# Performance work log

Hardware: AMD Instinct MI355X
Metric: run time of the kernel (lower is better)

The kernel has to match this reference:

```python
import jax, jax.numpy as jnp
import numpy as np

S, N, D, F, L = 16, 64, 1270, 150, 8  # sentences, entities, emb dim, ffnn_size, num_labels


def _xavier(key, shape):
    lim = np.sqrt(6.0 / (shape[0] + shape[1])).astype(np.float32)
    return jax.random.uniform(key, shape, jnp.float32, -lim, lim)


def setup_inputs() -> dict:
    key = jax.random.key(0)
    ks = jax.random.split(key, 8)
    entity_emb = jax.random.normal(ks[0], (S, N, D), jnp.float32)
    entity_scores = jax.random.normal(ks[1], (S, N), jnp.float32)
    rel_labels = jax.random.randint(ks[2], (S, N, N), 0, L)
    num_predicted_entities = jax.random.randint(ks[3], (S,), 0, N)
    # Linear params stored [in, out] (y = x @ W + b), transpose of torch layout.
    W_in = _xavier(ks[4], (3 * D, F))
    b_in = jnp.zeros((F,), jnp.float32)
    W_h = _xavier(ks[5], (F, F))
    b_h = jnp.zeros((F,), jnp.float32)
    W_out = _xavier(ks[6], (F, L - 1))
    b_out = jnp.zeros((L - 1,), jnp.float32)
    return {
        "entity_emb": entity_emb,
        "entity_scores": entity_scores,
        "W_in": W_in, "b_in": b_in,
        "W_h": W_h, "b_h": b_h,
        "W_out": W_out, "b_out": b_out,
        "rel_labels": rel_labels,
        "num_predicted_entities": num_predicted_entities,
    }


def reference(entity_emb, entity_scores, W_in, b_in, W_h, b_h, W_out, b_out,
              rel_labels, num_predicted_entities):
    s, n, d = entity_emb.shape
    # pair_emb = concat([e1_tiled, e2_tiled, e1*e2]) @ W_in  ==  split-weight fused form
    # (avoids materializing the [S,N,N,3D] tensor; same math).
    W1, W2, W3 = W_in[:d], W_in[d:2 * d], W_in[2 * d:]
    h = (jnp.einsum('sid,df->sif', entity_emb, W1)[:, :, None, :]
         + jnp.einsum('sjd,df->sjf', entity_emb, W2)[:, None, :, :]
         + jnp.einsum('sid,sjd,df->sijf', entity_emb, entity_emb, W3)
         + b_in)  # [S,N,N,F]
    # NOTE: original applies two more Linear layers with NO nonlinearity between them.
    h = h @ W_h + b_h
    scores = h @ W_out + b_out  # [S,N,N,L-1]
    # dropout is identity at inference (reference baseline)
    rel = scores + entity_scores[:, :, None, None] + entity_scores[:, None, :, None]
    dummy = jnp.zeros((s, n, n, 1), rel.dtype)
    rel_scores = jnp.concatenate([dummy, rel], axis=3)  # [S,N,N,L]
    # per-element cross entropy (reduction='none'), then pair mask, then sum
    logp = jax.nn.log_softmax(rel_scores, axis=-1)
    ce = -jnp.take_along_axis(logp, rel_labels[..., None], axis=-1)[..., 0]  # [S,N,N]
    ent_mask = jnp.arange(n)[None, :] < num_predicted_entities[:, None]  # [S,N]
    pair_mask = ent_mask[:, :, None] & ent_mask[:, None, :]  # [S,N,N]
    loss = jnp.sum(jnp.where(pair_mask, ce, jnp.zeros((), ce.dtype)))
    return rel_scores, loss
```

## Files before the change

### kernel.cpp

```cpp
#include <hip/hip_runtime.h>
#include <hip/hip_bf16.h>
#include <stdint.h>

typedef __attribute__((ext_vector_type(8))) short bf16x8;
typedef __attribute__((ext_vector_type(16))) float f32x16;

#define S_ 16
#define N_ 64
#define D_ 1270
#define F_ 150
#define KP_ 1280
#define FP_ 160
#define NKT 80
#define LOSS_OFF (S_*N_*N_*8)

#define HSTR 172

__device__ inline short f2b(float x) {
    union { float f; uint32_t u; } v; v.f = x;
    uint32_t r = (v.u + 0x7fffu + ((v.u >> 16) & 1u)) >> 16;
    return (short)r;
}
__device__ inline bf16x8 as_bf16x8(uint4 u) {
    union { uint4 a; bf16x8 b; } c; c.a = u; return c.b;
}

__global__ void k_pack(const float* __restrict__ emb, const float* __restrict__ win,
                       const float* __restrict__ wh, const float* __restrict__ wout,
                       short* __restrict__ eapk, short* __restrict__ w3pk,
                       short* __restrict__ w12pk, short* __restrict__ whpk,
                       short* __restrict__ wopk, float* __restrict__ out) {
    int t = blockIdx.x * 256 + threadIdx.x;
    if (t == 0) out[LOSS_OFF] = 0.f;
    const int TOT_EA = S_ * NKT * 2 * 64;
    const int NW3 = NKT * 5 * 64, NW12 = NKT * 10 * 64, NWH = 10 * 5 * 64, NWO = 10 * 64;
    if (t < TOT_EA) {
        int l  = t & 63;
        int mt = (t >> 6) & 1;
        int kt = (t >> 7) % NKT;
        int s  = t / (NKT * 2 * 64);
        int i  = (l & 31) + mt * 32;
        int k0 = kt * 16 + (l >> 5) * 8;
        const float* src = emb + (size_t)(s * N_ + i) * D_;
        bf16x8 pk;
        if (k0 + 8 <= D_) {
            float2 v0 = *(const float2*)(src + k0);
            float2 v1 = *(const float2*)(src + k0 + 2);
            float2 v2 = *(const float2*)(src + k0 + 4);
            float2 v3 = *(const float2*)(src + k0 + 6);
            pk[0]=f2b(v0.x); pk[1]=f2b(v0.y); pk[2]=f2b(v1.x); pk[3]=f2b(v1.y);
            pk[4]=f2b(v2.x); pk[5]=f2b(v2.y); pk[6]=f2b(v3.x); pk[7]=f2b(v3.y);
        } else {
            #pragma unroll
            for (int u = 0; u < 8; ++u) {
                int k = k0 + u;
                pk[u] = (k < D_) ? f2b(src[k]) : (short)0;
            }
        }
        *(bf16x8*)(eapk + (size_t)t * 8) = pk;
        return;
    }
    int t0 = t - TOT_EA;
    if (t0 < NW3) {
        int l = t0 & 63, nt = (t0 >> 6) % 5, kt = t0 / 320;
        int k0 = kt * 16 + (l >> 5) * 8, f = (l & 31) + nt * 32;
        bf16x8 pk;
        #pragma unroll
        for (int u = 0; u < 8; ++u) {
            int k = k0 + u;
            pk[u] = (k < D_ && f < F_) ? f2b(win[((size_t)(2 * D_) + k) * F_ + f]) : (short)0;
        }
        *(bf16x8*)(w3pk + (size_t)t0 * 8) = pk;
    } else if (t0 < NW3 + NW12) {
        int t2 = t0 - NW3;
        int l = t2 & 63, nt = (t2 >> 6) % 10, kt = t2 / 640;
        int k0 = kt * 16 + (l >> 5) * 8, c = (l & 31) + nt * 32;
        bf16x8 pk;
        #pragma unroll
        for (int u = 0; u < 8; ++u) {
            int k = k0 + u;
            float val = 0.f;
            if (k < D_) {
                if (c < FP_) { if (c < F_) val = win[(size_t)k * F_ + c]; }
                else { int f = c - FP_; if (f < F_) val = win[((size_t)D_ + k) * F_ + f]; }
            }
            pk[u] = f2b(val);
        }
        *(bf16x8*)(w12pk + (size_t)t2 * 8) = pk;
    } else if (t0 < NW3 + NW12 + NWH) {
        int t3 = t0 - NW3 - NW12;
        int l = t3 & 63, nt = (t3 >> 6) % 5, kt = t3 / 320;
        int k0 = kt * 16 + (l >> 5) * 8, f = (l & 31) + nt * 32;
        bf16x8 pk;
        #pragma unroll
        for (int u = 0; u < 8; ++u) {
            int k = k0 + u;
            pk[u] = (k < F_ && f < F_) ? f2b(wh[(size_t)k * F_ + f]) : (short)0;
        }
        *(bf16x8*)(whpk + (size_t)t3 * 8) = pk;
    } else if (t0 < NW3 + NW12 + NWH + NWO) {
        int t4 = t0 - NW3 - NW12 - NWH;
        int l = t4 & 63, kt = t4 >> 6;
        int k0 = kt * 16 + (l >> 5) * 8, f = l & 31;
        bf16x8 pk;
        #pragma unroll
        for (int u = 0; u < 8; ++u) {
            int k = k0 + u;
            pk[u] = (k < F_ && f < 7) ? f2b(wout[k * 7 + f]) : (short)0;
        }
        *(bf16x8*)(wopk + (size_t)t4 * 8) = pk;
    }
}

__global__ __launch_bounds__(128) void k_p12(const short* __restrict__ eapk,
                                             const short* __restrict__ w12pk,
                                             const float* __restrict__ bin,
                                             float* __restrict__ p1, float* __restrict__ p2) {
    __shared__ float red[16][64];
    int bid = blockIdx.x;
    int x = bid & 7, k = bid >> 3;
    int s = x * 2 + (k / 20);
    int rr = k % 20;
    int nt = rr >> 1, mt = rr & 1;
    int lane = threadIdx.x & 63, ks = threadIdx.x >> 6;
    f32x16 acc;
    #pragma unroll
    for (int r = 0; r < 16; ++r) acc[r] = 0.f;
    const size_t abase = (size_t)s * NKT * 2 * 64 * 8;
    #pragma unroll 8
    for (int kt = ks * 40; kt < ks * 40 + 40; ++kt) {
        bf16x8 a = *(const bf16x8*)(eapk + abase + ((size_t)kt * 2 + mt) * 64 * 8 + (size_t)lane * 8);
        bf16x8 b = *(const bf16x8*)(w12pk + ((size_t)(kt * 10 + nt) * 64 + lane) * 8);
        acc = __builtin_amdgcn_mfma_f32_32x32x16_bf16(a, b, acc, 0, 0, 0);
    }
    if (ks == 1) {
        #pragma unroll
        for (int r = 0; r < 16; ++r) red[r][lane] = acc[r];
    }
    __syncthreads();
    if (ks == 0) {
        int c = (lane & 31) + nt * 32;
        #pragma unroll
        for (int r = 0; r < 16; ++r) {
            float v = acc[r] + red[r][lane];
            int i = (r & 3) + 8 * (r >> 2) + 4 * (lane >> 5) + mt * 32;
            if (c < FP_) {
                p1[(size_t)(s * N_ + i) * FP_ + c] = v;
            } else {
                int f = c - FP_;
                float bv = (f < F_) ? bin[f] : 0.f;
                p2[(size_t)(s * N_ + i) * FP_ + f] = v + bv;
            }
        }
    }
}

template<int NB>
__device__ __forceinline__ void run_gemm1(const char* ea, const char* w3,
                                          const float* ej0, f32x16 (&acc)[3]) {
    uint4 euA, euB;
    uint4 bfA[3], bfB[3];
    float4 ejA[2], ejB4[2];

    auto fetch = [&](int kt, uint4& eu, uint4 (&bfv)[3], float4 (&ejr)[2]) {
        eu = *(const uint4*)(ea + (size_t)kt * 2048);
        #pragma unroll
        for (int nb = 0; nb < NB; ++nb)
            bfv[nb] = *(const uint4*)(w3 + (size_t)kt * 5120 + nb * 1024);
        ejr[0] = *(const float4*)(ej0 + kt * 16);
        ejr[1] = *(const float4*)(ej0 + kt * 16 + 4);
    };
    auto step = [&](const uint4& eu, const uint4 (&bfv)[3], const float4 (&ejr)[2]) {
        float ev[8] = {ejr[0].x,ejr[0].y,ejr[0].z,ejr[0].w,ejr[1].x,ejr[1].y,ejr[1].z,ejr[1].w};
        uint32_t ew[4] = {eu.x, eu.y, eu.z, eu.w};
        union { uint32_t u[4]; bf16x8 v; } av;
        #pragma unroll
        for (int p = 0; p < 4; ++p) {
            float flo = __uint_as_float(ew[p] << 16) * ev[2 * p];
            float fhi = __uint_as_float(ew[p] & 0xffff0000u) * ev[2 * p + 1];
            uint32_t pk;
            asm("v_cvt_pk_bf16_f32 %0, %1, %2" : "=v"(pk) : "v"(flo), "v"(fhi));
            av.u[p] = pk;
        }
        #pragma unroll
        for (int nb = 0; nb < NB; ++nb)
            acc[nb] = __builtin_amdgcn_mfma_f32_32x32x16_bf16(av.v, as_bf16x8(bfv[nb]), acc[nb], 0, 0, 0);
    };

    fetch(0, euA, bfA, ejA);
    fetch(1, euB, bfB, ejB4);
    #pragma unroll 1
    for (int kt = 0; kt < NKT; kt += 2) {
        step(euA, bfA, ejA);
        if (kt + 2 < NKT) fetch(kt + 2, euA, bfA, ejA);
        step(euB, bfB, ejB4);
        if (kt + 3 < NKT) fetch(kt + 3, euB, bfB, ejB4);
    }
}

template<int NB, int NT0>
__device__ __forceinline__ void write_h1(const f32x16 (&acc)[3], short* hBj,
                                         const float* p1s, const float* p2r,
                                         int lane, int mt) {
    #pragma unroll
    for (int nb = 0; nb < NB; ++nb) {
        const int f = (lane & 31) + (NT0 + nb) * 32;
        const float p2v = p2r[f];
        #pragma unroll
        for (int r = 0; r < 16; ++r) {
            int i = (r & 3) + 8 * (r >> 2) + 4 * (lane >> 5) + mt * 32;
            hBj[i * HSTR + f] = f2b(acc[nb][r] + p1s[(size_t)i * FP_ + f] + p2v);
        }
    }
}

__global__ __launch_bounds__(512, 1) void k_main(
    const float* __restrict__ emb, const float* __restrict__ esc,
    const short* __restrict__ eapk, const short* __restrict__ w3pk,
    const short* __restrict__ whpk, const short* __restrict__ wopk,
    const float* __restrict__ p1g, const float* __restrict__ p2g,
    const float* __restrict__ bhv, const float* __restrict__ bout,
    const int* __restrict__ labels, const int* __restrict__ nump,
    float* __restrict__ out) {

    __shared__ char lds[48128];
    float* sbuf = (float*)lds;
    float* ejB  = (float*)(lds + 4096);
    short* hB   = (short*)(lds + 4096);

    const int tid = threadIdx.x, lane = tid & 63, w = tid >> 6;
    const int jl = w & 1, mt = (w >> 1) & 1, nh = w >> 2;
    const int hi8 = (lane >> 5) << 3;
    const int bid = blockIdx.x;
    const int x = bid & 7, kk2 = bid >> 3;
    const int s = x * 2 + (kk2 >> 5);
    const int j0 = (kk2 & 31) * 2;

    for (int idx = tid; idx < 2 * KP_; idx += 512) {
        int jr = idx / KP_, k = idx - jr * KP_;
        ejB[idx] = (k < D_) ? emb[(size_t)(s * N_ + j0 + jr) * D_ + k] : 0.f;
    }
    __syncthreads();

    f32x16 acc[3];
    #pragma unroll
    for (int nb = 0; nb < 3; ++nb)
        #pragma unroll
        for (int r = 0; r < 16; ++r) acc[nb][r] = 0.f;

    {
        const char* ea = (const char*)eapk + (size_t)s * 163840 + mt * 1024 + lane * 16;
        const char* w3 = (const char*)w3pk + (nh ? 3 : 0) * 1024 + lane * 16;
        const float* ej0 = ejB + jl * KP_ + hi8;
        if (nh == 0) run_gemm1<3>(ea, w3, ej0, acc);
        else         run_gemm1<2>(ea, w3, ej0, acc);
    }
    __syncthreads();

    {
        const float* p1s = p1g + (size_t)(s * N_) * FP_;
        const float* p2r = p2g + (size_t)(s * N_ + j0 + jl) * FP_;
        short* hBj = hB + jl * (64 * HSTR);
        if (nh == 0) write_h1<3, 0>(acc, hBj, p1s, p2r, lane, mt);
        else         write_h1<2, 3>(acc, hBj, p1s, p2r, lane, mt);
    }
    __syncthreads();

    f32x16 acc2[3];
    #pragma unroll
    for (int c = 0; c < 3; ++c)
        #pragma unroll
        for (int r = 0; r < 16; ++r) acc2[c][r] = 0.f;
    #pragma unroll 1
    for (int kt = 0; kt < 10; ++kt) {
        #pragma unroll
        for (int c = 0; c < 3; ++c) {
            int t = w + 8 * c;
            if (t >= 20) break;
            int jl2 = t / 10, tt = t % 10;
            int mt2 = tt / 5, nt2 = tt % 5;
            const short* ap = hB + jl2 * (64 * HSTR) + ((lane & 31) + mt2 * 32) * HSTR
                            + kt * 16 + hi8;
            short4 alo = *(const short4*)ap;
            short4 ahi = *(const short4*)(ap + 4);
            union { short sh[8]; bf16x8 v; } av;
            av.sh[0] = alo.x; av.sh[1] = alo.y; av.sh[2] = alo.z; av.sh[3] = alo.w;
            av.sh[4] = ahi.x; av.sh[5] = ahi.y; av.sh[6] = ahi.z; av.sh[7] = ahi.w;
            bf16x8 b = *(const bf16x8*)(whpk + ((size_t)(kt * 5 + nt2) * 64 + lane) * 8);
            acc2[c] = __builtin_amdgcn_mfma_f32_32x32x16_bf16(av.v, b, acc2[c], 0, 0, 0);
        }
    }
    __syncthreads();

    #pragma unroll
    for (int c = 0; c < 3; ++c) {
        int t = w + 8 * c;
        if (t >= 20) break;
        int jl2 = t / 10, tt = t % 10;
        int mt2 = tt / 5, nt2 = tt % 5;
        int f = (lane & 31) + nt2 * 32;
        float bhf = (f < F_) ? bhv[f] : 0.f;
        #pragma unroll
        for (int r = 0; r < 16; ++r) {
            int i = (r & 3) + 8 * (r >> 2) + 4 * (lane >> 5) + mt2 * 32;
            short hv = (f < F_) ? f2b(acc2[c][r] + bhf) : (short)0;
            hB[jl2 * (64 * HSTR) + i * HSTR + f] = hv;
        }
    }
    __syncthreads();

    if (w < 4) {
        int jl3 = w >> 1, mt3 = w & 1;
        f32x16 acc3;
        #pragma unroll
        for (int r = 0; r < 16; ++r) acc3[r] = 0.f;
        #pragma unroll 1
        for (int kt = 0; kt < 10; ++kt) {
            const short* ap = hB + jl3 * (64 * HSTR) + ((lane & 31) + mt3 * 32) * HSTR
                            + kt * 16 + hi8;
            short4 alo = *(const short4*)ap;
            short4 ahi = *(const short4*)(ap + 4);
            union { short sh[8]; bf16x8 v; } av;
            av.sh[0] = alo.x; av.sh[1] = alo.y; av.sh[2] = alo.z; av.sh[3] = alo.w;
            av.sh[4] = ahi.x; av.sh[5] = ahi.y; av.sh[6] = ahi.z; av.sh[7] = ahi.w;
            bf16x8 b = *(const bf16x8*)(wopk + ((size_t)(kt * 64) + lane) * 8);
            acc3 = __builtin_amdgcn_mfma_f32_32x32x16_bf16(av.v, b, acc3, 0, 0, 0);
        }
        int c3 = lane & 31;
        if (c3 < 7) {
            float bo = bout[c3];
            #pragma unroll
            for (int r = 0; r < 16; ++r) {
                int i = (r & 3) + 8 * (r >> 2) + 4 * (lane >> 5) + mt3 * 32;
                sbuf[jl3 * 512 + i * 8 + c3] = acc3[r] + bo;
            }
        }
    }
    __syncthreads();

    if (tid < 128) {
        int jle = tid >> 6;
        int i = tid & 63;
        int j = j0 + jle;
        const float esi = esc[s * N_ + i];
        const float esj = esc[s * N_ + j];
        float rr[8];
        rr[0] = 0.f;
        #pragma unroll
        for (int l = 1; l < 8; ++l) rr[l] = sbuf[jle * 512 + i * 8 + (l - 1)] + esi + esj;

        float4* op = (float4*)(out + ((size_t)(s * N_ + i) * N_ + j) * 8);
        op[0] = make_float4(rr[0], rr[1], rr[2], rr[3]);
        op[1] = make_float4(rr[4], rr[5], rr[6], rr[7]);

        float m = rr[0];
        #pragma unroll
        for (int l = 1; l < 8; ++l) m = fmaxf(m, rr[l]);
        float sum = 0.f;
        #pragma unroll
        for (int l = 0; l < 8; ++l) sum += expf(rr[l] - m);
        const float lse = m + logf(sum);

        const int lab = labels[(s * N_ + i) * N_ + j];
        float ce = lse - rr[lab];
        const int np = nump[s];
        float v = (i < np && j < np) ? ce : 0.f;
        #pragma unroll
        for (int off = 32; off; off >>= 1) v += __shfl_down(v, off);
        if ((tid & 63) == 0) atomicAdd(out + LOSS_OFF, v);
    }
}

extern "C" void kernel_launch(void* const* d_in, const int* in_sizes, int n_in,
                              void* d_out, int out_size, void* d_ws, size_t ws_size,
                              hipStream_t stream) {
    const float* emb    = (const float*)d_in[0];
    const float* esc    = (const float*)d_in[1];
    const float* Win    = (const float*)d_in[2];
    const float* bin    = (const float*)d_in[3];
    const float* Wh     = (const float*)d_in[4];
    const float* bh     = (const float*)d_in[5];
    const float* Wout   = (const float*)d_in[6];
    const float* bout   = (const float*)d_in[7];
    const int*   labels = (const int*)d_in[8];
    const int*   nump   = (const int*)d_in[9];
    float* out = (float*)d_out;

    char* ws = (char*)d_ws;
    short* eapk  = (short*)(ws);
    short* w3pk  = (short*)(ws + 2621440);
    short* w12pk = (short*)(ws + 3031040);
    short* whpk  = (short*)(ws + 3850240);
    short* wopk  = (short*)(ws + 3901440);
    float* p1    = (float*)(ws + 3911680);
    float* p2    = (float*)(ws + 4567040);

    const int TOT_EA = S_ * NKT * 2 * 64;
    const int NW = NKT * 5 * 64 + NKT * 10 * 64 + 10 * 5 * 64 + 10 * 64;
    k_pack<<<(TOT_EA + NW + 255) / 256, 256, 0, stream>>>(emb, Win, Wh, Wout,
                                                          eapk, w3pk, w12pk, whpk, wopk, out);
    k_p12<<<320, 128, 0, stream>>>(eapk, w12pk, bin, p1, p2);
    k_main<<<S_ * 32, 512, 0, stream>>>(emb, esc, eapk, w3pk, whpk, wopk, p1, p2,
                                        bh, bout, labels, nump, out);
}
```

Before: 84.02 us.

## Stage GEMM1 operands through double-buffered LDS with async global_load_lds

Replaces the per-wave register-prefetched global loads of packed embeddings and W3 tiles in the first GEMM with block-cooperative asynchronous global-to-LDS copies, double-buffered over 20 super-steps of 4 k-tiles each. Each block loads every operand tile from global memory once and shares it across waves, instead of each wave fetching its own copy, which cuts redundant global/L2 traffic. In exchange LDS grows to about 66 KB, a block-wide barrier is added per super-step, and the MFMA operands are now read from LDS.

```diff
diff --git a/kernel.cpp b/kernel.cpp
--- a/kernel.cpp
+++ b/kernel.cpp
@@ -15,6 +15,7 @@
 #define LOSS_OFF (S_*N_*N_*8)
 
 #define HSTR 172
+#define STGB 28672
 
 __device__ inline short f2b(float x) {
     union { float f; uint32_t u; } v; v.f = x;
@@ -155,49 +156,6 @@
     }
 }
 
-template<int NB>
-__device__ __forceinline__ void run_gemm1(const char* ea, const char* w3,
-                                          const float* ej0, f32x16 (&acc)[3]) {
-    uint4 euA, euB;
-    uint4 bfA[3], bfB[3];
-    float4 ejA[2], ejB4[2];
-
-    auto fetch = [&](int kt, uint4& eu, uint4 (&bfv)[3], float4 (&ejr)[2]) {
-        eu = *(const uint4*)(ea + (size_t)kt * 2048);
-        #pragma unroll
-        for (int nb = 0; nb < NB; ++nb)
-            bfv[nb] = *(const uint4*)(w3 + (size_t)kt * 5120 + nb * 1024);
-        ejr[0] = *(const float4*)(ej0 + kt * 16);
-        ejr[1] = *(const float4*)(ej0 + kt * 16 + 4);
-    };
-    auto step = [&](const uint4& eu, const uint4 (&bfv)[3], const float4 (&ejr)[2]) {
-        float ev[8] = {ejr[0].x,ejr[0].y,ejr[0].z,ejr[0].w,ejr[1].x,ejr[1].y,ejr[1].z,ejr[1].w};
-        uint32_t ew[4] = {eu.x, eu.y, eu.z, eu.w};
-        union { uint32_t u[4]; bf16x8 v; } av;
-        #pragma unroll
-        for (int p = 0; p < 4; ++p) {
-            float flo = __uint_as_float(ew[p] << 16) * ev[2 * p];
-            float fhi = __uint_as_float(ew[p] & 0xffff0000u) * ev[2 * p + 1];
-            uint32_t pk;
-            asm("v_cvt_pk_bf16_f32 %0, %1, %2" : "=v"(pk) : "v"(flo), "v"(fhi));
-            av.u[p] = pk;
-        }
-        #pragma unroll
-        for (int nb = 0; nb < NB; ++nb)
-            acc[nb] = __builtin_amdgcn_mfma_f32_32x32x16_bf16(av.v, as_bf16x8(bfv[nb]), acc[nb], 0, 0, 0);
-    };
-
-    fetch(0, euA, bfA, ejA);
-    fetch(1, euB, bfB, ejB4);
-    #pragma unroll 1
-    for (int kt = 0; kt < NKT; kt += 2) {
-        step(euA, bfA, ejA);
-        if (kt + 2 < NKT) fetch(kt + 2, euA, bfA, ejA);
-        step(euB, bfB, ejB4);
-        if (kt + 3 < NKT) fetch(kt + 3, euB, bfB, ejB4);
-    }
-}
-
 template<int NB, int NT0>
 __device__ __forceinline__ void write_h1(const f32x16 (&acc)[3], short* hBj,
                                          const float* p1s, const float* p2r,
@@ -223,10 +181,11 @@
     const int* __restrict__ labels, const int* __restrict__ nump,
     float* __restrict__ out) {
 
-    __shared__ char lds[48128];
-    float* sbuf = (float*)lds;
-    float* ejB  = (float*)(lds + 4096);
-    short* hB   = (short*)(lds + 4096);
+    __shared__ char lds[67584];
+    float* ejB  = (float*)lds;
+    char*  stg  = lds + 10240;
+    short* hB   = (short*)lds;
+    float* sbuf = (float*)(lds + 44032);
 
     const int tid = threadIdx.x, lane = tid & 63, w = tid >> 6;
     const int jl = w & 1, mt = (w >> 1) & 1, nh = w >> 2;
@@ -236,10 +195,29 @@
     const int s = x * 2 + (kk2 >> 5);
     const int j0 = (kk2 & 31) * 2;
 
+    const char* easrc = (const char*)eapk + (size_t)s * 163840;
+    const char* w3src = (const char*)w3pk;
+
     for (int idx = tid; idx < 2 * KP_; idx += 512) {
         int jr = idx / KP_, k = idx - jr * KP_;
         ejB[idx] = (k < D_) ? emb[(size_t)(s * N_ + j0 + jr) * D_ + k] : 0.f;
     }
+
+    {
+        const char* ea = easrc;
+        const char* w3 = w3src;
+        #pragma unroll
+        for (int q = 0; q < 4; ++q) {
+            int n = w + 8 * q;
+            if (n < 28) {
+                const char* src = (n < 8) ? (ea + (n << 10)) : (w3 + ((n - 8) << 10));
+                __builtin_amdgcn_global_load_lds(
+                    (const __attribute__((address_space(1))) void*)(src + (lane << 4)),
+                    (__attribute__((address_space(3))) void*)(stg + (n << 10) + (lane << 4)),
+                    16, 0, 0);
+            }
+        }
+    }
     __syncthreads();
 
     f32x16 acc[3];
@@ -248,14 +226,57 @@
         #pragma unroll
         for (int r = 0; r < 16; ++r) acc[nb][r] = 0.f;
 
-    {
-        const char* ea = (const char*)eapk + (size_t)s * 163840 + mt * 1024 + lane * 16;
-        const char* w3 = (const char*)w3pk + (nh ? 3 : 0) * 1024 + lane * 16;
-        const float* ej0 = ejB + jl * KP_ + hi8;
-        if (nh == 0) run_gemm1<3>(ea, w3, ej0, acc);
-        else         run_gemm1<2>(ea, w3, ej0, acc);
-    }
-    __syncthreads();
+    const float* ejp = ejB + jl * KP_ + hi8;
+    const int NT0v = nh ? 3 : 0;
+    const int NBv  = nh ? 2 : 3;
+
+    #pragma unroll 1
+    for (int ss = 0; ss < 20; ++ss) {
+        const int cur = ss & 1;
+        if (ss < 19) {
+            const char* ea = easrc + (size_t)(ss + 1) * 8192;
+            const char* w3 = w3src + (size_t)(ss + 1) * 20480;
+            char* dst = stg + (cur ^ 1) * STGB;
+            #pragma unroll
+            for (int q = 0; q < 4; ++q) {
+                int n = w + 8 * q;
+                if (n < 28) {
+                    const char* src = (n < 8) ? (ea + (n << 10)) : (w3 + ((n - 8) << 10));
+                    __builtin_amdgcn_global_load_lds(
+                        (const __attribute__((address_space(1))) void*)(src + (lane << 4)),
+                        (__attribute__((address_space(3))) void*)(dst + (n << 10) + (lane << 4)),
+                        16, 0, 0);
+                }
+            }
+        }
+        const char* bb = stg + cur * STGB;
+        #pragma unroll
+        for (int kk = 0; kk < 4; ++kk) {
+            const int kt = ss * 4 + kk;
+            uint4 eu = *(const uint4*)(bb + kk * 2048 + mt * 1024 + (lane << 4));
+            float4 e0 = *(const float4*)(ejp + kt * 16);
+            float4 e1 = *(const float4*)(ejp + kt * 16 + 4);
+            float ev[8] = {e0.x,e0.y,e0.z,e0.w,e1.x,e1.y,e1.z,e1.w};
+            uint32_t ew[4] = {eu.x, eu.y, eu.z, eu.w};
+            union { uint32_t u[4]; bf16x8 v; } av;
+            #pragma unroll
+            for (int p = 0; p < 4; ++p) {
+                float flo = __uint_as_float(ew[p] << 16) * ev[2 * p];
+                float fhi = __uint_as_float(ew[p] & 0xffff0000u) * ev[2 * p + 1];
+                uint32_t pk;
+                asm("v_cvt_pk_bf16_f32 %0, %1, %2" : "=v"(pk) : "v"(flo), "v"(fhi));
+                av.u[p] = pk;
+            }
+            #pragma unroll
+            for (int nb = 0; nb < 3; ++nb) {
+                if (nb < NBv) {
+                    bf16x8 b8 = *(const bf16x8*)(bb + 8192 + kk * 5120 + (NT0v + nb) * 1024 + (lane << 4));
+                    acc[nb] = __builtin_amdgcn_mfma_f32_32x32x16_bf16(av.v, b8, acc[nb], 0, 0, 0);
+                }
+            }
+        }
+        __syncthreads();
+    }
 
     {
         const float* p1s = p1g + (size_t)(s * N_) * FP_;
```

Result: faster. 81.01 us (-3.6%).
